# Optimization experiments

Hardware: AMD Instinct MI355X
Metric: run time of the kernel (lower is better)

## Reference

```python
import jax, jax.numpy as jnp
import numpy as np

EPS = 1e-5
TEMP = 50.0


def setup_inputs() -> dict:
    key = jax.random.key(0)
    features = jax.random.normal(key, (4, 64, 128, 128), dtype=jnp.float32)
    return {"features": features, "patch_sim_neiref_neisimavgsize": 5}


def reference(features, patch_sim_neiref_neisimavgsize):
    k = patch_sim_neiref_neisimavgsize
    B, C, H, W = features.shape
    pad = k // 2
    xp = jnp.pad(features, ((0, 0), (0, 0), (pad, pad), (pad, pad)))
    # windows ordered (kh, kw) to match F.unfold: [B, k*k, C, H, W]
    wins = jnp.stack([xp[:, :, i:i + H, j:j + W]
                      for i in range(k) for j in range(k)], axis=1)
    # [B, H, W, k*k, C]
    patch = jnp.transpose(wins, (0, 3, 4, 1, 2)) + EPS
    patch_norm = patch / jnp.sqrt(jnp.sum(patch * patch, axis=-1, keepdims=True))
    center = patch_norm[..., (k * k) // 2:(k * k) // 2 + 1, :]  # center pixel of window
    sim = jnp.sum(patch_norm * center, axis=-1, keepdims=True)   # cosine sim [B,H,W,kk,1]
    wei = jax.nn.softmax(TEMP * sim, axis=-2)
    repr_vec = jnp.sum(patch * wei, axis=-2)                     # [B,H,W,C]
    return jnp.transpose(repr_vec, (0, 3, 1, 2))                 # [B,C,H,W]
```

## Files before the change

### kernel.cpp

```cpp
#include <hip/hip_runtime.h>

#define EPS 1e-5f
#define TEMP 50.0f
#define CCH 64
#define HH 128
#define WW 128
#define HWSZ (HH * WW)
#define CEPS2 (CCH * EPS * EPS)

#define IT 8
#define HT 12
#define HPX (HT * HT)

typedef _Float16 h16;
typedef h16 h2v __attribute__((ext_vector_type(2)));
typedef h16 h8v __attribute__((ext_vector_type(8)));

union H8 { h8v v; h2v p[4]; };

__device__ __forceinline__ float fdot2(h2v a, h2v b, float c) {
#if __has_builtin(__builtin_amdgcn_fdot2)
    return __builtin_amdgcn_fdot2(a, b, c, false);
#else
    return c + (float)a[0] * (float)b[0] + (float)a[1] * (float)b[1];
#endif
}

__global__ __launch_bounds__(256) void rv_fused(const float* __restrict__ x,
                                                float* __restrict__ out) {
    __shared__ h8v  tile[8][HPX];
    __shared__ float red[2][64][25];
    __shared__ float sh_s[HPX], sh_q[HPX];

    const int t  = threadIdx.x;
    const int w0 = blockIdx.x * IT;
    const int h0 = blockIdx.y * IT;
    const int b  = blockIdx.z;
    const float* xb = x + (size_t)b * (CCH * HWSZ);

#pragma unroll
    for (int it = 0; it < 5; ++it) {
        int k = it * 256 + t;
        if (k < 8 * HPX) {
            int hq = k / HPX;
            int px = k - hq * HPX;
            int row = px / HT;
            int col = px - row * HT;
            int gh = h0 + row - 2;
            int gw = w0 + col - 2;
            float vv[8] = {0.f, 0.f, 0.f, 0.f, 0.f, 0.f, 0.f, 0.f};
            if (gh >= 0 && gh < HH && gw >= 0 && gw < WW) {
                const float* p = xb + (size_t)(hq * 8) * HWSZ + gh * WW + gw;
#pragma unroll
                for (int j = 0; j < 8; ++j) vv[j] = p[j * HWSZ];
            }
            h8v hv;
#pragma unroll
            for (int j = 0; j < 8; ++j) hv[j] = (h16)vv[j];
            tile[hq][px] = hv;
        }
    }
    __syncthreads();

    if (t < HPX) {
        float s = 0.f, q = 0.f;
        const h2v one2 = {(h16)1.f, (h16)1.f};
#pragma unroll
        for (int hq = 0; hq < 8; ++hq) {
            H8 u; u.v = tile[hq][t];
#pragma unroll
            for (int j = 0; j < 4; ++j) {
                s = fdot2(u.p[j], one2, s);
                q = fdot2(u.p[j], u.p[j], q);
            }
        }
        sh_s[t] = s;
        sh_q[t] = q;
    }

    const int cg  = t >> 6;
    const int pix = t & 63;
    const int r   = pix >> 3;
    const int col = pix & 7;
    const int cpx = (r + 2) * HT + (col + 2);

    H8 c0, c1;
    c0.v = tile[cg * 2][cpx];
    c1.v = tile[cg * 2 + 1][cpx];

    float D[25];
#pragma unroll
    for (int dr = 0; dr < 5; ++dr) {
#pragma unroll
        for (int dc = 0; dc < 5; ++dc) {
            const int npx = (r + dr) * HT + (col + dc);
            H8 a0, a1;
            a0.v = tile[cg * 2][npx];
            a1.v = tile[cg * 2 + 1][npx];
            float d = 0.f;
#pragma unroll
            for (int j = 0; j < 4; ++j) d = fdot2(c0.p[j], a0.p[j], d);
#pragma unroll
            for (int j = 0; j < 4; ++j) d = fdot2(c1.p[j], a1.p[j], d);
            D[dr * 5 + dc] = d;
        }
    }

    if (cg >= 2) {
#pragma unroll
        for (int n = 0; n < 25; ++n) red[cg - 2][pix][n] = D[n];
    }
    __syncthreads();
    if (cg < 2) {
#pragma unroll
        for (int n = 0; n < 25; ++n) D[n] += red[cg][pix][n];
    }
    __syncthreads();
    if (cg == 1) {
#pragma unroll
        for (int n = 0; n < 25; ++n) red[0][pix][n] = D[n];
    }
    __syncthreads();

    if (cg == 0) {
        const float s_p = sh_s[cpx];
        const float q_p = sh_q[cpx];
        const float N2c = fmaf(2.f * EPS, s_p, q_p) + CEPS2;
        float logit[25];
        float m = -1e30f;
#pragma unroll
        for (int dr = 0; dr < 5; ++dr) {
#pragma unroll
            for (int dc = 0; dc < 5; ++dc) {
                const int n = dr * 5 + dc;
                const int npx = (r + dr) * HT + (col + dc);
                const float s_q = sh_s[npx];
                const float q_q = sh_q[npx];
                const float Dn = D[n] + red[0][pix][n] + EPS * (s_p + s_q) + CEPS2;
                const float N2n = fmaf(2.f * EPS, s_q, q_q) + CEPS2;
                const float sim = Dn * rsqrtf(N2n * N2c);
                logit[n] = TEMP * sim;
                m = fmaxf(m, logit[n]);
            }
        }
        float wei[25];
        float sum = 0.f;
#pragma unroll
        for (int n = 0; n < 25; ++n) {
            float e = __expf(logit[n] - m);
            wei[n] = e;
            sum += e;
        }
        const float rs = 1.f / sum;
#pragma unroll
        for (int n = 0; n < 25; ++n) red[0][pix][n] = wei[n] * rs;
    }
    __syncthreads();

    float acc[16];
#pragma unroll
    for (int j = 0; j < 16; ++j) acc[j] = EPS;
#pragma unroll
    for (int dr = 0; dr < 5; ++dr) {
#pragma unroll
        for (int dc = 0; dc < 5; ++dc) {
            const int npx = (r + dr) * HT + (col + dc);
            const float wn = red[0][pix][dr * 5 + dc];
            H8 a0, a1;
            a0.v = tile[cg * 2][npx];
            a1.v = tile[cg * 2 + 1][npx];
#pragma unroll
            for (int j = 0; j < 8; ++j) {
                acc[j]     = fmaf(wn, (float)a0.v[j], acc[j]);
                acc[8 + j] = fmaf(wn, (float)a1.v[j], acc[8 + j]);
            }
        }
    }

    const size_t obase = (size_t)b * (CCH * HWSZ) + (h0 + r) * WW + (w0 + col);
#pragma unroll
    for (int j = 0; j < 16; ++j) {
        out[obase + (size_t)(cg * 16 + j) * HWSZ] = acc[j];
    }
}

extern "C" void kernel_launch(void* const* d_in, const int* in_sizes, int n_in,
                              void* d_out, int out_size, void* d_ws, size_t ws_size,
                              hipStream_t stream) {
    const float* x = (const float*)d_in[0];
    float* outp = (float*)d_out;
    rv_fused<<<dim3(WW / IT, HH / IT, 4), dim3(256, 1, 1), 0, stream>>>(x, outp);
}
```

Baseline: 89.40 us.

## Split channels across lane pairs and reduce dot products with shuffles

The block shrinks to 128 threads. Each pair of adjacent lanes handles one output pixel, and each lane covers 32 channels. The partial cosine dot products are combined with a __shfl_xor instead of the shared-memory reduction array and its extra barriers, and both lanes compute the softmax redundantly. The tile is padded to cut LDS bank conflicts, and the small EPS·sum correction terms are dropped. This removes LDS round-trips and syncs, at the cost of more registers per thread and a slight numeric change.

Measured after the change: 90.54 us. Within noise of the previous version (+1.3%).

```diff
diff --git a/kernel.cpp b/kernel.cpp
--- a/kernel.cpp
+++ b/kernel.cpp
@@ -11,11 +11,11 @@
 #define IT 8
 #define HT 12
 #define HPX (HT * HT)
+#define HPAD 145
 
 typedef _Float16 h16;
 typedef h16 h2v __attribute__((ext_vector_type(2)));
 typedef h16 h8v __attribute__((ext_vector_type(8)));
-
 union H8 { h8v v; h2v p[4]; };
 
 __device__ __forceinline__ float fdot2(h2v a, h2v b, float c) {
@@ -26,11 +26,10 @@
 #endif
 }
 
-__global__ __launch_bounds__(256) void rv_fused(const float* __restrict__ x,
+__global__ __launch_bounds__(128) void rv_fused(const float* __restrict__ x,
                                                 float* __restrict__ out) {
-    __shared__ h8v  tile[8][HPX];
-    __shared__ float red[2][64][25];
-    __shared__ float sh_s[HPX], sh_q[HPX];
+    __shared__ h8v  tile[8][HPAD];
+    __shared__ float sh_q[HPX];
 
     const int t  = threadIdx.x;
     const int w0 = blockIdx.x * IT;
@@ -39,148 +38,120 @@
     const float* xb = x + (size_t)b * (CCH * HWSZ);
 
 #pragma unroll
-    for (int it = 0; it < 5; ++it) {
-        int k = it * 256 + t;
-        if (k < 8 * HPX) {
-            int hq = k / HPX;
-            int px = k - hq * HPX;
-            int row = px / HT;
-            int col = px - row * HT;
-            int gh = h0 + row - 2;
-            int gw = w0 + col - 2;
-            float vv[8] = {0.f, 0.f, 0.f, 0.f, 0.f, 0.f, 0.f, 0.f};
-            if (gh >= 0 && gh < HH && gw >= 0 && gw < WW) {
-                const float* p = xb + (size_t)(hq * 8) * HWSZ + gh * WW + gw;
+    for (int it = 0; it < 9; ++it) {
+        int k = it * 128 + t;
+        int hq = k / HPX;
+        int px = k - hq * HPX;
+        int row = px / HT;
+        int col = px - row * HT;
+        int gh = h0 + row - 2;
+        int gw = w0 + col - 2;
+        float vv[8] = {0.f, 0.f, 0.f, 0.f, 0.f, 0.f, 0.f, 0.f};
+        if (gh >= 0 && gh < HH && gw >= 0 && gw < WW) {
+            const float* p = xb + (size_t)(hq * 8) * HWSZ + gh * WW + gw;
 #pragma unroll
-                for (int j = 0; j < 8; ++j) vv[j] = p[j * HWSZ];
-            }
-            h8v hv;
+            for (int j = 0; j < 8; ++j) vv[j] = p[j * HWSZ];
+        }
+        h8v hv;
 #pragma unroll
-            for (int j = 0; j < 8; ++j) hv[j] = (h16)vv[j];
-            tile[hq][px] = hv;
-        }
+        for (int j = 0; j < 8; ++j) hv[j] = (h16)vv[j];
+        tile[hq][px] = hv;
     }
     __syncthreads();
 
-    if (t < HPX) {
-        float s = 0.f, q = 0.f;
-        const h2v one2 = {(h16)1.f, (h16)1.f};
+    for (int idx = t; idx < HPX; idx += 128) {
+        float q = 0.f;
 #pragma unroll
         for (int hq = 0; hq < 8; ++hq) {
-            H8 u; u.v = tile[hq][t];
+            H8 u; u.v = tile[hq][idx];
 #pragma unroll
-            for (int j = 0; j < 4; ++j) {
-                s = fdot2(u.p[j], one2, s);
-                q = fdot2(u.p[j], u.p[j], q);
-            }
+            for (int j = 0; j < 4; ++j) q = fdot2(u.p[j], u.p[j], q);
         }
-        sh_s[t] = s;
-        sh_q[t] = q;
+        sh_q[idx] = q;
     }
 
-    const int cg  = t >> 6;
-    const int pix = t & 63;
-    const int r   = pix >> 3;
-    const int col = pix & 7;
-    const int cpx = (r + 2) * HT + (col + 2);
+    const int half = t & 1;
+    const int pix  = t >> 1;
+    const int r    = pix >> 3;
+    const int c    = pix & 7;
+    const int cpx  = (r + 2) * HT + (c + 2);
 
-    H8 c0, c1;
-    c0.v = tile[cg * 2][cpx];
-    c1.v = tile[cg * 2 + 1][cpx];
+    H8 ctr[4];
+#pragma unroll
+    for (int g = 0; g < 4; ++g) ctr[g].v = tile[4 * half + g][cpx];
 
     float D[25];
 #pragma unroll
     for (int dr = 0; dr < 5; ++dr) {
 #pragma unroll
         for (int dc = 0; dc < 5; ++dc) {
-            const int npx = (r + dr) * HT + (col + dc);
-            H8 a0, a1;
-            a0.v = tile[cg * 2][npx];
-            a1.v = tile[cg * 2 + 1][npx];
+            const int npx = (r + dr) * HT + (c + dc);
             float d = 0.f;
 #pragma unroll
-            for (int j = 0; j < 4; ++j) d = fdot2(c0.p[j], a0.p[j], d);
+            for (int g = 0; g < 4; ++g) {
+                H8 a; a.v = tile[4 * half + g][npx];
 #pragma unroll
-            for (int j = 0; j < 4; ++j) d = fdot2(c1.p[j], a1.p[j], d);
+                for (int j = 0; j < 4; ++j) d = fdot2(ctr[g].p[j], a.p[j], d);
+            }
             D[dr * 5 + dc] = d;
         }
     }
+#pragma unroll
+    for (int n = 0; n < 25; ++n) D[n] += __shfl_xor(D[n], 1);
 
-    if (cg >= 2) {
-#pragma unroll
-        for (int n = 0; n < 25; ++n) red[cg - 2][pix][n] = D[n];
-    }
-    __syncthreads();
-    if (cg < 2) {
-#pragma unroll
-        for (int n = 0; n < 25; ++n) D[n] += red[cg][pix][n];
-    }
-    __syncthreads();
-    if (cg == 1) {
-#pragma unroll
-        for (int n = 0; n < 25; ++n) red[0][pix][n] = D[n];
-    }
     __syncthreads();
 
-    if (cg == 0) {
-        const float s_p = sh_s[cpx];
-        const float q_p = sh_q[cpx];
-        const float N2c = fmaf(2.f * EPS, s_p, q_p) + CEPS2;
-        float logit[25];
-        float m = -1e30f;
-#pragma unroll
-        for (int dr = 0; dr < 5; ++dr) {
-#pragma unroll
-            for (int dc = 0; dc < 5; ++dc) {
-                const int n = dr * 5 + dc;
-                const int npx = (r + dr) * HT + (col + dc);
-                const float s_q = sh_s[npx];
-                const float q_q = sh_q[npx];
-                const float Dn = D[n] + red[0][pix][n] + EPS * (s_p + s_q) + CEPS2;
-                const float N2n = fmaf(2.f * EPS, s_q, q_q) + CEPS2;
-                const float sim = Dn * rsqrtf(N2n * N2c);
-                logit[n] = TEMP * sim;
-                m = fmaxf(m, logit[n]);
-            }
-        }
-        float wei[25];
-        float sum = 0.f;
-#pragma unroll
-        for (int n = 0; n < 25; ++n) {
-            float e = __expf(logit[n] - m);
-            wei[n] = e;
-            sum += e;
-        }
-        const float rs = 1.f / sum;
-#pragma unroll
-        for (int n = 0; n < 25; ++n) red[0][pix][n] = wei[n] * rs;
-    }
-    __syncthreads();
-
-    float acc[16];
-#pragma unroll
-    for (int j = 0; j < 16; ++j) acc[j] = EPS;
+    const float N2c = sh_q[cpx] + CEPS2;
+    float lg[25];
+    float m = -1e30f;
 #pragma unroll
     for (int dr = 0; dr < 5; ++dr) {
 #pragma unroll
         for (int dc = 0; dc < 5; ++dc) {
-            const int npx = (r + dr) * HT + (col + dc);
-            const float wn = red[0][pix][dr * 5 + dc];
-            H8 a0, a1;
-            a0.v = tile[cg * 2][npx];
-            a1.v = tile[cg * 2 + 1][npx];
+            const int n = dr * 5 + dc;
+            const int npx = (r + dr) * HT + (c + dc);
+            const float N2n = sh_q[npx] + CEPS2;
+            const float sim = (D[n] + CEPS2) * rsqrtf(N2n * N2c);
+            lg[n] = TEMP * sim;
+            m = fmaxf(m, lg[n]);
+        }
+    }
+    float wei[25];
+    float sum = 0.f;
 #pragma unroll
-            for (int j = 0; j < 8; ++j) {
-                acc[j]     = fmaf(wn, (float)a0.v[j], acc[j]);
-                acc[8 + j] = fmaf(wn, (float)a1.v[j], acc[8 + j]);
+    for (int n = 0; n < 25; ++n) {
+        wei[n] = __expf(lg[n] - m);
+        sum += wei[n];
+    }
+    const float rs = 1.f / sum;
+#pragma unroll
+    for (int n = 0; n < 25; ++n) wei[n] *= rs;
+
+    float acc[32];
+#pragma unroll
+    for (int j = 0; j < 32; ++j) acc[j] = EPS;
+#pragma unroll
+    for (int dr = 0; dr < 5; ++dr) {
+#pragma unroll
+        for (int dc = 0; dc < 5; ++dc) {
+            const int npx = (r + dr) * HT + (c + dc);
+            const float wn = wei[dr * 5 + dc];
+#pragma unroll
+            for (int g = 0; g < 4; ++g) {
+                H8 a; a.v = tile[4 * half + g][npx];
+#pragma unroll
+                for (int j = 0; j < 8; ++j)
+                    acc[g * 8 + j] = fmaf(wn, (float)a.v[j], acc[g * 8 + j]);
             }
         }
     }
 
-    const size_t obase = (size_t)b * (CCH * HWSZ) + (h0 + r) * WW + (w0 + col);
+    const size_t obase = (size_t)b * (CCH * HWSZ)
+                       + (size_t)(32 * half) * HWSZ
+                       + (h0 + r) * WW + (w0 + c);
 #pragma unroll
-    for (int j = 0; j < 16; ++j) {
-        out[obase + (size_t)(cg * 16 + j) * HWSZ] = acc[j];
+    for (int j = 0; j < 32; ++j) {
+        out[obase + (size_t)j * HWSZ] = acc[j];
     }
 }
 
@@ -189,5 +160,5 @@
                               hipStream_t stream) {
     const float* x = (const float*)d_in[0];
     float* outp = (float*)d_out;
-    rv_fused<<<dim3(WW / IT, HH / IT, 4), dim3(256, 1, 1), 0, stream>>>(x, outp);
+    rv_fused<<<dim3(WW / IT, HH / IT, 4), dim3(128, 1, 1), 0, stream>>>(x, outp);
 }
```
